# Optimization experiments

Measured on AMD Instinct MI355X. Metric: run time of the kernel, lower is better.

## Reference

```python
import jax, jax.numpy as jnp
import numpy as np

B, N, D = 8, 256, 128   # batch, nodes, feature width
MID, OUT = 128, 128
FEAT = 2 * D            # concat(n_features, hidden)


def _glorot(key, fan_in, fan_out):
    s = (2.0 / (fan_in + fan_out)) ** 0.5
    return jax.random.normal(key, (fan_in, fan_out), dtype=jnp.float32) * s


def setup_inputs() -> dict:
    key = jax.random.key(0)
    ks = jax.random.split(key, 12)
    inp = {
        "hidden": jax.random.normal(ks[0], (B, N, D), dtype=jnp.float32),
        "n_features": jax.random.normal(ks[1], (B, N, D), dtype=jnp.float32),
        "e_features": jax.random.normal(ks[2], (B, N, N, D), dtype=jnp.float32),
        "g_features": jax.random.normal(ks[3], (B, D), dtype=jnp.float32),
        "adj": jax.random.bernoulli(ks[4], 0.5, (B, N, N)).astype(jnp.float32),
        # Linear params (haiku Linear: y = x @ w + b)
        "W1": _glorot(ks[5], FEAT, MID), "b1": jnp.zeros((MID,), jnp.float32),
        "W2": _glorot(ks[6], FEAT, MID), "b2": jnp.zeros((MID,), jnp.float32),
        "We": _glorot(ks[7], D, MID),    "be": jnp.zeros((MID,), jnp.float32),
        "Wg": _glorot(ks[8], D, MID),    "bg": jnp.zeros((MID,), jnp.float32),
        "Wo1": _glorot(ks[9], FEAT, OUT), "bo1": jnp.zeros((OUT,), jnp.float32),
        "Wo2": _glorot(ks[10], MID, OUT), "bo2": jnp.zeros((OUT,), jnp.float32),
    }
    return inp


def reference(hidden, n_features, e_features, g_features, adj,
              W1, b1, W2, b2, We, be, Wg, bg, Wo1, bo1, Wo2, bo2):
    # features: (B, N, 2D)
    features = jnp.concatenate([n_features, hidden], axis=-1)
    msg_1 = features @ W1 + b1              # (B, N, MID)
    msg_2 = features @ W2 + b2              # (B, N, MID)
    msg_e = e_features @ We + be            # (B, N, N, MID)
    msg_g = g_features @ Wg + bg            # (B, MID)
    # broadcast-add: msgs[b, i, j] = msg_1[b, j] + msg_2[b, i] + msg_e[b, i, j] + msg_g[b]
    msgs = (msg_1[:, None, :, :] + msg_2[:, :, None, :]
            + msg_e + msg_g[:, None, None, :])  # (B, N, N, MID)
    # masked max reduction over axis=1 (default reduction=jnp.max branch)
    msgs = jnp.max(msgs * adj[..., None], axis=1)  # (B, N, MID)
    ret = (features @ Wo1 + bo1) + (msgs @ Wo2 + bo2)  # (B, N, OUT)
    return ret
```

## Files before the change

### kernel.cpp

```cpp
#include <hip/hip_runtime.h>
#include <stdint.h>

#define B_   8
#define N_   256
#define D_   128
#define MID_ 128
#define FEAT_ 256

typedef __attribute__((ext_vector_type(4))) float  floatx4;
typedef __attribute__((ext_vector_type(8))) __bf16 bf16x8;

__device__ __forceinline__ floatx4 mfma16(bf16x8 a, bf16x8 b, floatx4 c) {
    return __builtin_amdgcn_mfma_f32_16x16x32_bf16(a, b, c, 0, 0, 0);
}

__device__ __forceinline__ bf16x8 cvt8(floatx4 a, floatx4 b) {
    bf16x8 r;
    r[0] = (__bf16)a[0]; r[1] = (__bf16)a[1]; r[2] = (__bf16)a[2]; r[3] = (__bf16)a[3];
    r[4] = (__bf16)b[0]; r[5] = (__bf16)b[1]; r[6] = (__bf16)b[2]; r[7] = (__bf16)b[3];
    return r;
}

__global__ void __launch_bounds__(256)
kA(const float* __restrict__ nfeat, const float* __restrict__ hidden,
   const float* __restrict__ W1, const float* __restrict__ W2,
   const float* __restrict__ Wo1,
   const float* __restrict__ g, const float* __restrict__ Wg,
   const float* __restrict__ bg, const float* __restrict__ b1,
   const float* __restrict__ be, const float* __restrict__ b2,
   const float* __restrict__ bo1, const float* __restrict__ bo2,
   float* __restrict__ C, float* __restrict__ msg2, float* __restrict__ retA) {
    __shared__ __bf16 Wb[8 * 8 * 64 * 8];
    __shared__ float gp_part[2][MID_];
    __shared__ float gp_sh[MID_];
    int t = threadIdx.x;
    int wid = blockIdx.y;
    const float* W = (wid == 0) ? W1 : ((wid == 1) ? W2 : Wo1);
    for (int idx = t; idx < 32768; idx += 256) {
        int k = idx >> 7, m = idx & 127;
        Wb[(((k >> 5) * 8 + (m >> 4)) * 64 + ((k >> 3) & 3) * 16 + (m & 15)) * 8 + (k & 7)]
            = (__bf16)W[idx];
    }
    int bblk = blockIdx.x >> 2;
    if (wid == 0) {
        int m = t & 127, h = t >> 7;
        const float* gr = g + bblk * D_;
        float a = 0.f;
        for (int k = h * 64; k < h * 64 + 64; ++k)
            a += gr[k] * Wg[k * MID_ + m];
        gp_part[h][m] = a;
    }
    __syncthreads();
    if (wid == 0 && t < 128)
        gp_sh[t] = gp_part[0][t] + gp_part[1][t] + bg[t] + b1[t] + be[t];
    __syncthreads();

    int lane = t & 63, w = t >> 6;
    int n16 = lane & 15, quad = lane >> 4;
    int R = blockIdx.x * 64 + w * 16 + n16;
    const float* frow0 = nfeat  + (size_t)R * D_ + quad * 8;
    const float* frow1 = hidden + (size_t)R * D_ + quad * 8;

    bf16x8 bfrag[8];
#pragma unroll
    for (int ks = 0; ks < 8; ++ks) {
        const float* p = (ks < 4) ? (frow0 + ks * 32) : (frow1 + (ks - 4) * 32);
        floatx4 v0 = *(const floatx4*)p;
        floatx4 v1 = *(const floatx4*)(p + 4);
        bfrag[ks] = cvt8(v0, v1);
    }

    float* outp = (wid == 0) ? C : ((wid == 1) ? msg2 : retA);
#pragma unroll 2
    for (int mt = 0; mt < 8; ++mt) {
        floatx4 acc = (floatx4)0.f;
#pragma unroll
        for (int ks = 0; ks < 8; ++ks) {
            bf16x8 a = *(const bf16x8*)&Wb[((ks * 8 + mt) * 64 + lane) * 8];
            acc = mfma16(a, bfrag[ks], acc);
        }
        int m0 = mt * 16 + quad * 4;
        floatx4 add;
        if (wid == 0)      add = *(const floatx4*)&gp_sh[m0];
        else if (wid == 1) add = *(const floatx4*)&b2[m0];
        else {
            floatx4 x = *(const floatx4*)&bo1[m0];
            floatx4 y = *(const floatx4*)&bo2[m0];
            add = x + y;
        }
        *(floatx4*)&outp[(size_t)R * MID_ + m0] = acc + add;
    }
}

__global__ void __launch_bounds__(256, 4)
kB(const float* __restrict__ e, const float* __restrict__ We,
   const float* __restrict__ adj, const float* __restrict__ C,
   const float* __restrict__ msg2, const float* __restrict__ retA,
   const float* __restrict__ Wo2, float* __restrict__ out) {
    __shared__ __bf16 Wb[4 * 8 * 64 * 8];
    __shared__ float C_sh[MID_];
    __shared__ float wmax[4][MID_];
    __shared__ float msgs_sh[MID_];
    __shared__ float part[2][MID_];
    __shared__ unsigned short list_sh[N_];
    __shared__ float aval_sh[N_];
    __shared__ int wcnt[4];

    int t = threadIdx.x;
    int b = blockIdx.x >> 8, j = blockIdx.x & 255;
    int lane = t & 63, w = t >> 6;

    for (int idx = t; idx < 16384; idx += 256) {
        int k = idx >> 7, m = idx & 127;
        Wb[(((k >> 5) * 8 + (m >> 4)) * 64 + ((k >> 3) & 3) * 16 + (m & 15)) * 8 + (k & 7)]
            = (__bf16)We[idx];
    }
    float av = adj[(size_t)b * N_ * N_ + (size_t)t * N_ + j];
    bool act = (av != 0.f);
    unsigned long long mk = __ballot(act);
    if (lane == 0) wcnt[w] = __popcll(mk);
    if (t < 128) C_sh[t] = C[((size_t)b * N_ + j) * MID_ + t];
    __syncthreads();
    int nact = wcnt[0] + wcnt[1] + wcnt[2] + wcnt[3];
    int base = 0;
    if (w > 0) base += wcnt[0];
    if (w > 1) base += wcnt[1];
    if (w > 2) base += wcnt[2];
    int pos = base + __popcll(mk & ((1ull << lane) - 1ull));
    if (act) { list_sh[pos] = (unsigned short)t; aval_sh[pos] = av; }
    __syncthreads();

    int n16 = lane & 15, quad = lane >> 4;
    const size_t erow = (size_t)N_ * D_;
    const float* ebase = e + (size_t)b * N_ * N_ * D_ + (size_t)j * D_ + quad * 8;
    const float* m2b   = msg2 + (size_t)b * N_ * MID_;

    floatx4 rm[8];
#pragma unroll
    for (int mt = 0; mt < 8; ++mt) rm[mt] = (floatx4)(-INFINITY);

    int nchunks = (nact + 15) >> 4;
    for (int c = w; c < nchunks; c += 4) {
        int slot = c * 16 + n16;
        int idx = 0; float aw = 0.f;
        if (slot < nact) { idx = list_sh[slot]; aw = aval_sh[slot]; }
        const float* rowp = ebase + (size_t)idx * erow;
        floatx4 v0[4], v1[4];
#pragma unroll
        for (int q = 0; q < 4; ++q) {
            v0[q] = *(const floatx4*)(rowp + q * 32);
            v1[q] = *(const floatx4*)(rowp + q * 32 + 4);
        }
        bf16x8 ef[4];
#pragma unroll
        for (int q = 0; q < 4; ++q) ef[q] = cvt8(v0[q], v1[q]);
        const float* m2r = m2b + (size_t)idx * MID_;
#pragma unroll 2
        for (int mt = 0; mt < 8; ++mt) {
            int m0 = mt * 16 + quad * 4;
            floatx4 acc = *(const floatx4*)&C_sh[m0];
#pragma unroll
            for (int ks = 0; ks < 4; ++ks) {
                bf16x8 aW = *(const bf16x8*)&Wb[((ks * 8 + mt) * 64 + lane) * 8];
                acc = mfma16(aW, ef[ks], acc);
            }
            floatx4 m2v = *(const floatx4*)&m2r[m0];
#pragma unroll
            for (int r = 0; r < 4; ++r)
                rm[mt][r] = fmaxf(rm[mt][r], (acc[r] + m2v[r]) * aw);
        }
    }

#pragma unroll
    for (int mt = 0; mt < 8; ++mt) {
#pragma unroll
        for (int r = 0; r < 4; ++r) {
            float v = rm[mt][r];
            v = fmaxf(v, __shfl_xor(v, 1, 64));
            v = fmaxf(v, __shfl_xor(v, 2, 64));
            v = fmaxf(v, __shfl_xor(v, 4, 64));
            v = fmaxf(v, __shfl_xor(v, 8, 64));
            rm[mt][r] = v;
        }
    }
    if (n16 == 0) {
#pragma unroll
        for (int mt = 0; mt < 8; ++mt)
            *(floatx4*)&wmax[w][mt * 16 + quad * 4] = rm[mt];
    }
    __syncthreads();

    int m = t & 127, h = t >> 7;
    if (t < 128) {
        float mx = fmaxf(fmaxf(wmax[0][m], wmax[1][m]), fmaxf(wmax[2][m], wmax[3][m]));
        if (nact < 256) mx = fmaxf(mx, 0.f);
        msgs_sh[m] = mx;
    }
    __syncthreads();

    float a2 = 0.f;
    for (int k = h * 64; k < h * 64 + 64; ++k)
        a2 += msgs_sh[k] * Wo2[k * MID_ + m];
    part[h][m] = a2;
    __syncthreads();
    if (t < 128) {
        int R = b * N_ + j;
        out[(size_t)R * MID_ + m] = retA[R * MID_ + m] + part[0][m] + part[1][m];
    }
}

extern "C" void kernel_launch(void* const* d_in, const int* in_sizes, int n_in,
                              void* d_out, int out_size, void* d_ws, size_t ws_size,
                              hipStream_t stream) {
    (void)in_sizes; (void)n_in; (void)out_size; (void)ws_size;
    const float* hidden = (const float*)d_in[0];
    const float* nfeat  = (const float*)d_in[1];
    const float* e      = (const float*)d_in[2];
    const float* g      = (const float*)d_in[3];
    const float* adj    = (const float*)d_in[4];
    const float* W1  = (const float*)d_in[5];
    const float* b1  = (const float*)d_in[6];
    const float* W2  = (const float*)d_in[7];
    const float* b2  = (const float*)d_in[8];
    const float* We  = (const float*)d_in[9];
    const float* be  = (const float*)d_in[10];
    const float* Wg  = (const float*)d_in[11];
    const float* bg  = (const float*)d_in[12];
    const float* Wo1 = (const float*)d_in[13];
    const float* bo1 = (const float*)d_in[14];
    const float* Wo2 = (const float*)d_in[15];
    const float* bo2 = (const float*)d_in[16];
    float* outp = (float*)d_out;

    float* ws   = (float*)d_ws;
    float* C    = ws;
    float* msg2 = C + 262144;
    float* retA = msg2 + 262144;

    kA<<<dim3(32, 3), 256, 0, stream>>>(nfeat, hidden, W1, W2, Wo1,
                                        g, Wg, bg, b1, be, b2, bo1, bo2,
                                        C, msg2, retA);
    kB<<<2048, 256, 0, stream>>>(e, We, adj, C, msg2, retA, Wo2, outp);
}
```

Baseline: 414.6 us.

## Pre-swizzle bf16 weights once and process two output columns per block

A new small kernel converts W1, W2, Wo1 and We to bf16 in the MFMA fragment layout once, so kA and kB copy packed bf16 into shared memory with vector loads instead of converting and scattering fp32 per block. kB now handles two j columns per block (half the grid), amortizing the We staging over twice the work. It also processes two 16-row chunks per iteration to raise memory-level parallelism. The cost is an extra launch, more registers per thread in kB, and fewer blocks to hide latency.

```diff
diff --git a/kernel.cpp b/kernel.cpp
--- a/kernel.cpp
+++ b/kernel.cpp
@@ -8,6 +8,7 @@
 #define FEAT_ 256
 
 typedef __attribute__((ext_vector_type(4))) float  floatx4;
+typedef __attribute__((ext_vector_type(4))) int    intx4;
 typedef __attribute__((ext_vector_type(8))) __bf16 bf16x8;
 
 __device__ __forceinline__ floatx4 mfma16(bf16x8 a, bf16x8 b, floatx4 c) {
@@ -22,9 +23,27 @@
 }
 
 __global__ void __launch_bounds__(256)
+kW(const float* __restrict__ W1, const float* __restrict__ W2,
+   const float* __restrict__ Wo1, const float* __restrict__ We,
+   __bf16* __restrict__ dst) {
+    int t = threadIdx.x;
+    int g = blockIdx.x * 2 + (t >> 7);
+    int m = t & 127;
+    const float* src; int kg; int off;
+    if (g < 32)      { src = W1;  kg = g;      off = 0; }
+    else if (g < 64) { src = W2;  kg = g - 32; off = 32768; }
+    else if (g < 96) { src = Wo1; kg = g - 64; off = 65536; }
+    else             { src = We;  kg = g - 96; off = 98304; }
+    bf16x8 r;
+#pragma unroll
+    for (int jv = 0; jv < 8; ++jv) r[jv] = (__bf16)src[(kg * 8 + jv) * MID_ + m];
+    int base = (((kg >> 2) * 8 + (m >> 4)) * 64 + (kg & 3) * 16 + (m & 15)) * 8;
+    *(bf16x8*)&dst[off + base] = r;
+}
+
+__global__ void __launch_bounds__(256)
 kA(const float* __restrict__ nfeat, const float* __restrict__ hidden,
-   const float* __restrict__ W1, const float* __restrict__ W2,
-   const float* __restrict__ Wo1,
+   const __bf16* __restrict__ Wpre,
    const float* __restrict__ g, const float* __restrict__ Wg,
    const float* __restrict__ bg, const float* __restrict__ b1,
    const float* __restrict__ be, const float* __restrict__ b2,
@@ -35,11 +54,11 @@
     __shared__ float gp_sh[MID_];
     int t = threadIdx.x;
     int wid = blockIdx.y;
-    const float* W = (wid == 0) ? W1 : ((wid == 1) ? W2 : Wo1);
-    for (int idx = t; idx < 32768; idx += 256) {
-        int k = idx >> 7, m = idx & 127;
-        Wb[(((k >> 5) * 8 + (m >> 4)) * 64 + ((k >> 3) & 3) * 16 + (m & 15)) * 8 + (k & 7)]
-            = (__bf16)W[idx];
+    {
+        const intx4* srcW = (const intx4*)(Wpre + (size_t)wid * 32768);
+        intx4* dstW = (intx4*)Wb;
+#pragma unroll
+        for (int it = 0; it < 16; ++it) dstW[t + it * 256] = srcW[t + it * 256];
     }
     int bblk = blockIdx.x >> 2;
     if (wid == 0) {
@@ -93,7 +112,7 @@
 }
 
 __global__ void __launch_bounds__(256, 4)
-kB(const float* __restrict__ e, const float* __restrict__ We,
+kB(const float* __restrict__ e, const __bf16* __restrict__ Wes,
    const float* __restrict__ adj, const float* __restrict__ C,
    const float* __restrict__ msg2, const float* __restrict__ retA,
    const float* __restrict__ Wo2, float* __restrict__ out) {
@@ -107,105 +126,124 @@
     __shared__ int wcnt[4];
 
     int t = threadIdx.x;
-    int b = blockIdx.x >> 8, j = blockIdx.x & 255;
+    int b = blockIdx.x >> 7, j0 = (blockIdx.x & 127) << 1;
     int lane = t & 63, w = t >> 6;
-
-    for (int idx = t; idx < 16384; idx += 256) {
-        int k = idx >> 7, m = idx & 127;
-        Wb[(((k >> 5) * 8 + (m >> 4)) * 64 + ((k >> 3) & 3) * 16 + (m & 15)) * 8 + (k & 7)]
-            = (__bf16)We[idx];
-    }
-    float av = adj[(size_t)b * N_ * N_ + (size_t)t * N_ + j];
-    bool act = (av != 0.f);
-    unsigned long long mk = __ballot(act);
-    if (lane == 0) wcnt[w] = __popcll(mk);
-    if (t < 128) C_sh[t] = C[((size_t)b * N_ + j) * MID_ + t];
-    __syncthreads();
-    int nact = wcnt[0] + wcnt[1] + wcnt[2] + wcnt[3];
-    int base = 0;
-    if (w > 0) base += wcnt[0];
-    if (w > 1) base += wcnt[1];
-    if (w > 2) base += wcnt[2];
-    int pos = base + __popcll(mk & ((1ull << lane) - 1ull));
-    if (act) { list_sh[pos] = (unsigned short)t; aval_sh[pos] = av; }
-    __syncthreads();
-
     int n16 = lane & 15, quad = lane >> 4;
+
+    {
+        const intx4* srcW = (const intx4*)Wes;
+        intx4* dstW = (intx4*)Wb;
+#pragma unroll
+        for (int it = 0; it < 8; ++it) dstW[t + it * 256] = srcW[t + it * 256];
+    }
+    float2 av2 = *(const float2*)&adj[(size_t)b * N_ * N_ + (size_t)t * N_ + j0];
+
     const size_t erow = (size_t)N_ * D_;
-    const float* ebase = e + (size_t)b * N_ * N_ * D_ + (size_t)j * D_ + quad * 8;
-    const float* m2b   = msg2 + (size_t)b * N_ * MID_;
-
-    floatx4 rm[8];
-#pragma unroll
-    for (int mt = 0; mt < 8; ++mt) rm[mt] = (floatx4)(-INFINITY);
-
-    int nchunks = (nact + 15) >> 4;
-    for (int c = w; c < nchunks; c += 4) {
-        int slot = c * 16 + n16;
-        int idx = 0; float aw = 0.f;
-        if (slot < nact) { idx = list_sh[slot]; aw = aval_sh[slot]; }
-        const float* rowp = ebase + (size_t)idx * erow;
-        floatx4 v0[4], v1[4];
-#pragma unroll
-        for (int q = 0; q < 4; ++q) {
-            v0[q] = *(const floatx4*)(rowp + q * 32);
-            v1[q] = *(const floatx4*)(rowp + q * 32 + 4);
-        }
-        bf16x8 ef[4];
-#pragma unroll
-        for (int q = 0; q < 4; ++q) ef[q] = cvt8(v0[q], v1[q]);
-        const float* m2r = m2b + (size_t)idx * MID_;
+    const float* m2b = msg2 + (size_t)b * N_ * MID_;
+
+    for (int jj = 0; jj < 2; ++jj) {
+        int j = j0 + jj;
+        float av = jj ? av2.y : av2.x;
+        bool act = (av != 0.f);
+        unsigned long long mk = __ballot(act);
+        if (lane == 0) wcnt[w] = __popcll(mk);
+        if (t < 128) C_sh[t] = C[((size_t)b * N_ + j) * MID_ + t];
+        __syncthreads();
+        int nact = wcnt[0] + wcnt[1] + wcnt[2] + wcnt[3];
+        int base = 0;
+        if (w > 0) base += wcnt[0];
+        if (w > 1) base += wcnt[1];
+        if (w > 2) base += wcnt[2];
+        int pos = base + __popcll(mk & ((1ull << lane) - 1ull));
+        if (act) { list_sh[pos] = (unsigned short)t; aval_sh[pos] = av; }
+        __syncthreads();
+
+        const float* ebase = e + (size_t)b * N_ * N_ * D_ + (size_t)j * D_ + quad * 8;
+
+        floatx4 rm[8];
+#pragma unroll
+        for (int mt = 0; mt < 8; ++mt) rm[mt] = (floatx4)(-INFINITY);
+
+        int nch = (nact + 15) >> 4;
+        for (int c = w; c < nch; c += 8) {
+            int s0 = c * 16 + n16;
+            int s1 = (c + 4) * 16 + n16;
+            int i0 = 0, i1 = 0; float aw0 = 0.f, aw1 = 0.f;
+            if (s0 < nact) { i0 = list_sh[s0]; aw0 = aval_sh[s0]; }
+            if (s1 < nact) { i1 = list_sh[s1]; aw1 = aval_sh[s1]; }
+            const float* r0 = ebase + (size_t)i0 * erow;
+            const float* r1 = ebase + (size_t)i1 * erow;
+            bf16x8 ef0[4], ef1[4];
+#pragma unroll
+            for (int q = 0; q < 4; ++q) {
+                floatx4 a0 = *(const floatx4*)(r0 + q * 32);
+                floatx4 b0 = *(const floatx4*)(r0 + q * 32 + 4);
+                floatx4 a1 = *(const floatx4*)(r1 + q * 32);
+                floatx4 b1 = *(const floatx4*)(r1 + q * 32 + 4);
+                ef0[q] = cvt8(a0, b0);
+                ef1[q] = cvt8(a1, b1);
+            }
+            const float* m2r0 = m2b + (size_t)i0 * MID_;
+            const float* m2r1 = m2b + (size_t)i1 * MID_;
 #pragma unroll 2
+            for (int mt = 0; mt < 8; ++mt) {
+                int m0 = mt * 16 + quad * 4;
+                floatx4 c4 = *(const floatx4*)&C_sh[m0];
+                floatx4 acc0 = c4, acc1 = c4;
+#pragma unroll
+                for (int ks = 0; ks < 4; ++ks) {
+                    bf16x8 aW = *(const bf16x8*)&Wb[((ks * 8 + mt) * 64 + lane) * 8];
+                    acc0 = mfma16(aW, ef0[ks], acc0);
+                    acc1 = mfma16(aW, ef1[ks], acc1);
+                }
+                floatx4 m20 = *(const floatx4*)&m2r0[m0];
+                floatx4 m21 = *(const floatx4*)&m2r1[m0];
+#pragma unroll
+                for (int r = 0; r < 4; ++r) {
+                    float v0 = (acc0[r] + m20[r]) * aw0;
+                    float v1 = (acc1[r] + m21[r]) * aw1;
+                    rm[mt][r] = fmaxf(rm[mt][r], fmaxf(v0, v1));
+                }
+            }
+        }
+
+#pragma unroll
         for (int mt = 0; mt < 8; ++mt) {
-            int m0 = mt * 16 + quad * 4;
-            floatx4 acc = *(const floatx4*)&C_sh[m0];
-#pragma unroll
-            for (int ks = 0; ks < 4; ++ks) {
-                bf16x8 aW = *(const bf16x8*)&Wb[((ks * 8 + mt) * 64 + lane) * 8];
-                acc = mfma16(aW, ef[ks], acc);
+#pragma unroll
+            for (int r = 0; r < 4; ++r) {
+                float v = rm[mt][r];
+                v = fmaxf(v, __shfl_xor(v, 1, 64));
+                v = fmaxf(v, __shfl_xor(v, 2, 64));
+                v = fmaxf(v, __shfl_xor(v, 4, 64));
+                v = fmaxf(v, __shfl_xor(v, 8, 64));
+                rm[mt][r] = v;
             }
-            floatx4 m2v = *(const floatx4*)&m2r[m0];
-#pragma unroll
-            for (int r = 0; r < 4; ++r)
-                rm[mt][r] = fmaxf(rm[mt][r], (acc[r] + m2v[r]) * aw);
-        }
-    }
-
-#pragma unroll
-    for (int mt = 0; mt < 8; ++mt) {
-#pragma unroll
-        for (int r = 0; r < 4; ++r) {
-            float v = rm[mt][r];
-            v = fmaxf(v, __shfl_xor(v, 1, 64));
-            v = fmaxf(v, __shfl_xor(v, 2, 64));
-            v = fmaxf(v, __shfl_xor(v, 4, 64));
-            v = fmaxf(v, __shfl_xor(v, 8, 64));
-            rm[mt][r] = v;
-        }
-    }
-    if (n16 == 0) {
-#pragma unroll
-        for (int mt = 0; mt < 8; ++mt)
-            *(floatx4*)&wmax[w][mt * 16 + quad * 4] = rm[mt];
-    }
-    __syncthreads();
-
-    int m = t & 127, h = t >> 7;
-    if (t < 128) {
-        float mx = fmaxf(fmaxf(wmax[0][m], wmax[1][m]), fmaxf(wmax[2][m], wmax[3][m]));
-        if (nact < 256) mx = fmaxf(mx, 0.f);
-        msgs_sh[m] = mx;
-    }
-    __syncthreads();
-
-    float a2 = 0.f;
-    for (int k = h * 64; k < h * 64 + 64; ++k)
-        a2 += msgs_sh[k] * Wo2[k * MID_ + m];
-    part[h][m] = a2;
-    __syncthreads();
-    if (t < 128) {
-        int R = b * N_ + j;
-        out[(size_t)R * MID_ + m] = retA[R * MID_ + m] + part[0][m] + part[1][m];
+        }
+        if (n16 == 0) {
+#pragma unroll
+            for (int mt = 0; mt < 8; ++mt)
+                *(floatx4*)&wmax[w][mt * 16 + quad * 4] = rm[mt];
+        }
+        __syncthreads();
+
+        int m = t & 127, h = t >> 7;
+        if (t < 128) {
+            float mx = fmaxf(fmaxf(wmax[0][m], wmax[1][m]), fmaxf(wmax[2][m], wmax[3][m]));
+            if (nact < 256) mx = fmaxf(mx, 0.f);
+            msgs_sh[m] = mx;
+        }
+        __syncthreads();
+
+        float a2 = 0.f;
+        for (int k = h * 64; k < h * 64 + 64; ++k)
+            a2 += msgs_sh[k] * Wo2[k * MID_ + m];
+        part[h][m] = a2;
+        __syncthreads();
+        if (t < 128) {
+            int R = b * N_ + j;
+            out[(size_t)R * MID_ + m] = retA[R * MID_ + m] + part[0][m] + part[1][m];
+        }
+        __syncthreads();
     }
 }
 
@@ -232,13 +270,15 @@
     const float* bo2 = (const float*)d_in[16];
     float* outp = (float*)d_out;
 
-    float* ws   = (float*)d_ws;
-    float* C    = ws;
+    float* ws = (float*)d_ws;
+    __bf16* Wpre = (__bf16*)ws;
+    float* C    = ws + 57344;
     float* msg2 = C + 262144;
     float* retA = msg2 + 262144;
 
-    kA<<<dim3(32, 3), 256, 0, stream>>>(nfeat, hidden, W1, W2, Wo1,
+    kW<<<56, 256, 0, stream>>>(W1, W2, Wo1, We, Wpre);
+    kA<<<dim3(32, 3), 256, 0, stream>>>(nfeat, hidden, Wpre,
                                         g, Wg, bg, b1, be, b2, bo1, bo2,
                                         C, msg2, retA);
-    kB<<<2048, 256, 0, stream>>>(e, We, adj, C, msg2, retA, Wo2, outp);
-}
+    kB<<<1024, 256, 0, stream>>>(e, Wpre + 98304, adj, C, msg2, retA, Wo2, outp);
+}
```

Result: slower. 428.2 us (+3.3%).
